# Kernel optimization log

Hardware: AMD Instinct MI355X
Metric: run time of the kernel (lower is better)

Reference implementation:

```python
import jax, jax.numpy as jnp
import numpy as np

SCALE = 1.0 / 4.0      # alpha / dim
MULTIPLIER = 1.0

def _act(h):
    return jax.nn.gelu(h, approximate=False)  # torch nn.GELU(approximate='none')

def setup_inputs() -> dict:
    key = jax.random.key(0)
    ks = jax.random.split(key, 9)
    B, T, D = 64, 77, 768
    N, R = 1024, 4
    return {
        "x":     jax.random.normal(ks[0], (B, T, D), jnp.float32),
        "W_org": jax.random.normal(ks[1], (D, D), jnp.float32) * 0.02,
        "b_org": jax.random.normal(ks[2], (D,), jnp.float32) * 0.02,
        "w1":    jax.random.normal(ks[3], (N, D, R), jnp.float32) * 0.02,
        "b1":    jax.random.normal(ks[4], (N, R), jnp.float32) * 0.02,
        "mid_w": jax.random.normal(ks[5], (N, R, R), jnp.float32) * 0.02,
        "mid_b": jax.random.normal(ks[6], (N, R), jnp.float32) * 0.02,
        "w_out": jax.random.normal(ks[7], (N, R, D), jnp.float32) * 0.02,
        "b_out": jax.random.normal(ks[8], (N, D), jnp.float32) * 0.02,
    }

def reference(x, W_org, b_org, w1, b1, mid_w, mid_b, w_out, b_out):
    # per-concept low-rank MLP: h in [B, T, N, R]
    h = jnp.einsum('btd,ndh->btnh', x, w1) + b1[None, None]
    h = _act(h)
    # repeated 'h' in 'nhh' takes the diagonal of mid_w (elementwise scale),
    # exactly matching torch.einsum semantics in the source.
    h = jnp.einsum('btnh,nhh->btnh', h, mid_w) + mid_b[None, None]
    h = _act(h)
    # fuse out-projection with sum over concepts: sum_n (h_n @ w_out_n) + sum_n b_out_n
    up = jnp.einsum('btnh,nhd->btd', h, w_out) + jnp.sum(b_out, axis=0)
    org = x @ W_org.T + b_org
    return org + up * (MULTIPLIER * SCALE)
```

## Files before the change

kernel.cpp:

```cpp
#include <hip/hip_runtime.h>
#include <hip/hip_bf16.h>

#define M_TOK 4928
#define M_PAD 5120
#define D_DIM 768
#define NR    4096
#define K_CAT 4864
#define KT_ALL 152

typedef __bf16 bf16;
typedef __attribute__((ext_vector_type(8))) __bf16 bf16x8;
typedef __attribute__((ext_vector_type(4))) float f32x4;
typedef __attribute__((address_space(1))) uint32_t gu32;
typedef __attribute__((address_space(3))) uint32_t su32;

#define GLDS(P, LDSP) \
  __builtin_amdgcn_global_load_lds((gu32*)(P), (su32*)(LDSP), 16, 0, 0)

__device__ __forceinline__ float act_fast(float v) {
  float e = __builtin_amdgcn_exp2f(v * -2.4554677f);
  return v * __builtin_amdgcn_rcpf(1.0f + e);
}

__device__ __forceinline__ int xcd_swizzle(int orig, int nwg) {
  const int q = nwg >> 3, r = nwg & 7;
  const int x = orig & 7, rest = orig >> 3;
  return (x < r ? x * (q + 1) : r * (q + 1) + (x - r) * q) + rest;
}


__global__ __launch_bounds__(256) void k_prep_x(const float* __restrict__ x,
                                                bf16* __restrict__ Xb) {
  int idx = (blockIdx.x * 256 + threadIdx.x) * 4;
  if (idx >= M_PAD * D_DIM) return;
  int m = idx / D_DIM;
  union { uint2 u; bf16 h[4]; } o;
  if (m < M_TOK) {
    float4 v = *(const float4*)(x + idx);
    o.h[0] = (bf16)v.x; o.h[1] = (bf16)v.y; o.h[2] = (bf16)v.z; o.h[3] = (bf16)v.w;
  } else {
    o.h[0] = o.h[1] = o.h[2] = o.h[3] = (bf16)0.0f;
  }
  *(uint2*)(Xb + idx) = o.u;
}

__global__ __launch_bounds__(256) void k_prep_w1t(const float* __restrict__ w1,
                                                  bf16* __restrict__ W1t) {
  int gid = blockIdx.x * 256 + threadIdx.x;
  int n = gid / 96, oct = gid % 96;
  const float4* src = (const float4*)w1 + (size_t)n * D_DIM + oct * 8;
  bf16x8 rows[4];
#pragma unroll
  for (int d = 0; d < 8; ++d) {
    float4 v = src[d];
    rows[0][d] = (bf16)v.x; rows[1][d] = (bf16)v.y;
    rows[2][d] = (bf16)v.z; rows[3][d] = (bf16)v.w;
  }
  size_t base = (size_t)n * 4 * D_DIM + oct * 8;
#pragma unroll
  for (int r = 0; r < 4; ++r)
    *(bf16x8*)(W1t + base + (size_t)r * D_DIM) = rows[r];
}

__global__ __launch_bounds__(256) void k_prep_w2t_t(const float* __restrict__ w_out,
                                                    bf16* __restrict__ W2t) {
  __shared__ float S[64 * 65];
  const int bk = blockIdx.x & 63, bd = blockIdx.x >> 6;
  const int k0 = bk * 64, d0 = bd * 64;
  const int tr = threadIdx.x >> 4;
  const int tc = (threadIdx.x & 15) * 4;
#pragma unroll
  for (int p = 0; p < 4; ++p) {
    const int kr = tr + p * 16;
    float4 v = *(const float4*)(w_out + (size_t)(k0 + kr) * D_DIM + d0 + tc);
    S[kr * 65 + tc + 0] = v.x; S[kr * 65 + tc + 1] = v.y;
    S[kr * 65 + tc + 2] = v.z; S[kr * 65 + tc + 3] = v.w;
  }
  __syncthreads();
#pragma unroll
  for (int p = 0; p < 4; ++p) {
    const int dr = tr + p * 16;
    union { uint2 u; bf16 h[4]; } o;
#pragma unroll
    for (int i = 0; i < 4; ++i) o.h[i] = (bf16)(0.25f * S[(tc + i) * 65 + dr]);
    *(uint2*)(W2t + (size_t)(d0 + dr) * K_CAT + k0 + tc) = o.u;
  }
}

__global__ __launch_bounds__(256) void k_prep_w2t_org(const float* __restrict__ W_org,
                                                      bf16* __restrict__ W2t) {
  int idx = (blockIdx.x * 256 + threadIdx.x) * 4;
  if (idx >= D_DIM * D_DIM) return;
  int d = idx / D_DIM, c = idx % D_DIM;
  float4 v = *(const float4*)(W_org + idx);
  union { uint2 u; bf16 h[4]; } o;
  o.h[0] = (bf16)v.x; o.h[1] = (bf16)v.y; o.h[2] = (bf16)v.z; o.h[3] = (bf16)v.w;
  *(uint2*)(W2t + (size_t)d * K_CAT + NR + c) = o.u;
}

__global__ __launch_bounds__(256) void k_bias_partial(const float* __restrict__ b_out,
                                                      float* __restrict__ partial) {
  int b = blockIdx.x;
  for (int d = threadIdx.x; d < D_DIM; d += 256) {
    float s = 0.0f;
    for (int n = b * 32; n < b * 32 + 32; ++n) s += b_out[n * D_DIM + d];
    partial[b * D_DIM + d] = s;
  }
}

__global__ __launch_bounds__(256) void k_bias_final2(const float* __restrict__ partial,
                                                     const float* __restrict__ b_org,
                                                     const float* __restrict__ mid_w,
                                                     float* __restrict__ bias_total,
                                                     float* __restrict__ diag) {
  int b = blockIdx.x;
  if (b < 3) {
    int d = b * 256 + threadIdx.x;
    if (d >= D_DIM) return;
    float s = 0.0f;
#pragma unroll
    for (int p = 0; p < 32; ++p) s += partial[p * D_DIM + d];
    bias_total[d] = b_org[d] + 0.25f * s;
  } else {
    int j = (b - 3) * 256 + threadIdx.x;
    diag[j] = mid_w[(j >> 2) * 16 + (j & 3) * 5];
  }
}


__device__ __forceinline__ int swz_slot(int kg, int lr) {
  return (kg ^ ((lr >> 1) & 3)) << 3;
}

__device__ __forceinline__ void stage_unit8(const bf16* g, int ld, int row0, int col0,
                                            bf16* lds) {
  const int lane = threadIdx.x & 63;
  const int wave = threadIdx.x >> 6;
  const int src_slot = (lane & 3) ^ ((lane >> 3) & 3);
#pragma unroll
  for (int c = 0; c < 2; ++c) {
    const int chunk = wave * 2 + c;
    const int row = row0 + chunk * 16 + (lane >> 2);
    const bf16* gp = g + (size_t)row * ld + col0 + (src_slot << 3);
    GLDS(gp, lds + chunk * 512);
  }
}

#define TILE_E (128 * 32)


#define G1_IT(S_, DO_STG, LAST_)                                                \
  {                                                                             \
    if (LAST_) { asm volatile("s_waitcnt vmcnt(0)" ::: "memory"); }             \
    else       { asm volatile("s_waitcnt vmcnt(4)" ::: "memory"); }             \
    asm volatile("s_barrier" ::: "memory");                                     \
    bf16x8 a_[4], b_[4];                                                        \
    _Pragma("unroll") for (int i = 0; i < 4; ++i)                               \
      a_[i] = *(const bf16x8*)(&As[S_][aOff + i * 512]);                        \
    _Pragma("unroll") for (int j = 0; j < 4; ++j)                               \
      b_[j] = *(const bf16x8*)(&Bs[S_][bOff + j * 512]);                        \
    if (DO_STG) {                                                               \
      GLDS(aP0, &As[((S_) + 2) % 3][ldsC0]);                                    \
      GLDS(aP1, &As[((S_) + 2) % 3][ldsC1]);                                    \
      GLDS(bP0, &Bs[((S_) + 2) % 3][ldsC0]);                                    \
      GLDS(bP1, &Bs[((S_) + 2) % 3][ldsC1]);                                    \
      aP0 += 32; aP1 += 32; bP0 += 32; bP1 += 32;                               \
    }                                                                           \
    _Pragma("unroll") for (int i = 0; i < 4; ++i)                               \
      _Pragma("unroll") for (int j = 0; j < 4; ++j)                             \
        acc[i][j] = __builtin_amdgcn_mfma_f32_16x16x32_bf16(b_[j], a_[i], acc[i][j], 0, 0, 0); \
  }

__global__ __launch_bounds__(256) void k_gemm1(const bf16* __restrict__ Xb,
                                               const bf16* __restrict__ W1t,
                                               bf16* __restrict__ H2,
                                               const float* __restrict__ b1,
                                               const float* __restrict__ diag,
                                               const float* __restrict__ midb) {
  __shared__ bf16 As[3][TILE_E];
  __shared__ bf16 Bs[3][TILE_E];
  const int wgid = xcd_swizzle(blockIdx.x, 39 * 32);
  const int bmt = wgid >> 5;
  const int bnt = wgid & 31;
  const int m0 = bmt * 128, n0 = bnt * 128;
  const int lane = threadIdx.x & 63;
  const int wave = threadIdx.x >> 6;
  const int wm = wave >> 1, wn = wave & 1;
  const int lr = lane & 15, kg = lane >> 4;
  const int slot = swz_slot(kg, lr);
  const int aOff = (wm * 64 + lr) * 32 + slot;
  const int bOff = (wn * 64 + lr) * 32 + slot;

  const int src_slot = (lane & 3) ^ ((lane >> 3) & 3);
  const int srow = (wave * 2) * 16 + (lane >> 2);
  const bf16* aP0 = Xb  + (size_t)(m0 + srow) * D_DIM + (src_slot << 3);
  const bf16* aP1 = aP0 + 16 * D_DIM;
  const bf16* bP0 = W1t + (size_t)(n0 + srow) * D_DIM + (src_slot << 3);
  const bf16* bP1 = bP0 + 16 * D_DIM;
  const int ldsC0 = (wave * 2) * 512, ldsC1 = ldsC0 + 512;

  f32x4 acc[4][4];
#pragma unroll
  for (int i = 0; i < 4; ++i)
#pragma unroll
    for (int j = 0; j < 4; ++j) acc[i][j] = (f32x4)(0.0f);

  GLDS(aP0, &As[0][ldsC0]); GLDS(aP1, &As[0][ldsC1]);
  GLDS(bP0, &Bs[0][ldsC0]); GLDS(bP1, &Bs[0][ldsC1]);
  aP0 += 32; aP1 += 32; bP0 += 32; bP1 += 32;
  GLDS(aP0, &As[1][ldsC0]); GLDS(aP1, &As[1][ldsC1]);
  GLDS(bP0, &Bs[1][ldsC0]); GLDS(bP1, &Bs[1][ldsC1]);
  aP0 += 32; aP1 += 32; bP0 += 32; bP1 += 32;

  for (int g = 0; g < 7; ++g) {
    G1_IT(0, true, false)
    G1_IT(1, true, false)
    G1_IT(2, true, false)
  }
  G1_IT(0, true, false)
  G1_IT(1, false, false)
  G1_IT(2, false, true)

#pragma unroll
  for (int j = 0; j < 4; ++j) {
    const int jcb = n0 + wn * 64 + j * 16 + kg * 4;
    const float4 b1v = *(const float4*)(b1 + jcb);
    const float4 dgv = *(const float4*)(diag + jcb);
    const float4 mbv = *(const float4*)(midb + jcb);
#pragma unroll
    for (int i = 0; i < 4; ++i) {
      const int mr = m0 + wm * 64 + i * 16 + lr;
      union { uint2 u; bf16 h[4]; } o;
      float h;
      h = act_fast(acc[i][j][0] + b1v.x); o.h[0] = (bf16)act_fast(h * dgv.x + mbv.x);
      h = act_fast(acc[i][j][1] + b1v.y); o.h[1] = (bf16)act_fast(h * dgv.y + mbv.y);
      h = act_fast(acc[i][j][2] + b1v.z); o.h[2] = (bf16)act_fast(h * dgv.z + mbv.z);
      h = act_fast(acc[i][j][3] + b1v.w); o.h[3] = (bf16)act_fast(h * dgv.w + mbv.w);
      *(uint2*)(H2 + (size_t)mr * NR + jcb) = o.u;
    }
  }
}


#define ENGINE(KT0, KT1, STAGE_A, STAGE_B)                                      \
  {                                                                             \
    STAGE_A((KT0) + 0, 0); STAGE_B((KT0) + 0, 0);                               \
    STAGE_A((KT0) + 1, 1); STAGE_B((KT0) + 1, 1);                               \
    STAGE_A((KT0) + 2, 2); STAGE_B((KT0) + 2, 2);                               \
    asm volatile("s_waitcnt vmcnt(8)" ::: "memory");                            \
    asm volatile("s_barrier" ::: "memory");                                     \
    for (int t = (KT0); t < (KT1); ++t) {                                       \
      const int s  = (t - (KT0)) & 3;                                           \
      const int st = (t - (KT0) + 3) & 3;                                       \
      const bool more = (t + 3 < (KT1));                                        \
      bf16x8 a[8], b[4];                                                        \
      _Pragma("unroll") for (int i = 0; i < 4; ++i)                             \
        a[i] = *(const bf16x8*)(As[s] + aBase + i * 512);                       \
      _Pragma("unroll") for (int j = 0; j < 4; ++j)                             \
        b[j] = *(const bf16x8*)(Bs[s] + bBase + j * 512);                       \
      if (more) { STAGE_A(t + 3, st); }                                         \
      asm volatile("s_barrier" ::: "memory");                                   \
      __builtin_amdgcn_s_setprio(1);                                            \
      _Pragma("unroll") for (int i = 0; i < 4; ++i)                             \
        _Pragma("unroll") for (int j = 0; j < 4; ++j)                           \
          acc[i][j] = __builtin_amdgcn_mfma_f32_16x16x32_bf16(b[j], a[i], acc[i][j], 0, 0, 0); \
      __builtin_amdgcn_s_setprio(0);                                            \
      asm volatile("s_barrier" ::: "memory");                                   \
      _Pragma("unroll") for (int i = 0; i < 4; ++i)                             \
        a[4 + i] = *(const bf16x8*)(As[s] + aBase + 2048 + i * 512);            \
      if (more) { STAGE_B(t + 3, st); }                                         \
      {                                                                         \
        int ahead = ((KT1) - 1) - (t + 1);                                      \
        if (ahead >= 2)      { asm volatile("s_waitcnt vmcnt(8)" ::: "memory"); } \
        else if (ahead == 1) { asm volatile("s_waitcnt vmcnt(4)" ::: "memory"); } \
        else                 { asm volatile("s_waitcnt vmcnt(0)" ::: "memory"); } \
      }                                                                         \
      asm volatile("s_barrier" ::: "memory");                                   \
      __builtin_amdgcn_s_setprio(1);                                            \
      _Pragma("unroll") for (int i = 0; i < 4; ++i)                             \
        _Pragma("unroll") for (int j = 0; j < 4; ++j)                           \
          acc[4 + i][j] = __builtin_amdgcn_mfma_f32_16x16x32_bf16(b[j], a[4 + i], acc[4 + i][j], 0, 0, 0); \
      __builtin_amdgcn_s_setprio(0);                                            \
      asm volatile("s_barrier" ::: "memory");                                   \
    }                                                                           \
  }

template <int SPLITS>
__global__ __launch_bounds__(512) void k_gemm2(const bf16* __restrict__ H2,
                                               const bf16* __restrict__ Xb,
                                               const bf16* __restrict__ W2t,
                                               void* __restrict__ outp,
                                               const float* __restrict__ bias) {
  __shared__ bf16 As[4][8192];
  __shared__ bf16 Bs[4][8192];
  const int nwg = 20 * 3 * SPLITS;
  const int wgid = xcd_swizzle(blockIdx.x, nwg);
  const int bmt = wgid / (3 * SPLITS);
  const int rem = wgid % (3 * SPLITS);
  const int ks  = rem / 3;
  const int bnt = rem % 3;
  const int m0 = bmt * 256, n0 = bnt * 256;
  const int lane = threadIdx.x & 63;
  const int wave = threadIdx.x >> 6;
  const int wm = wave >> 2, wn = wave & 3;
  const int lr = lane & 15, kg = lane >> 4;
  const int slotE = swz_slot(kg, lr);
  const int aBase = (wm * 128 + lr) * 32 + slotE;
  const int bBase = (wn * 64 + lr) * 32 + slotE;
  constexpr int KT_PER = KT_ALL / SPLITS;
  const int kt0 = ks * KT_PER, kt1 = kt0 + KT_PER;

  f32x4 acc[8][4];
#pragma unroll
  for (int i = 0; i < 8; ++i)
#pragma unroll
    for (int j = 0; j < 4; ++j) acc[i][j] = (f32x4)(0.0f);

#define G2_SA(kt, buf)                                                  \
  {                                                                     \
    const int k0s = (kt) * 32;                                          \
    if (k0s < NR) stage_unit8(H2, NR, m0, k0s, As[(buf)]);              \
    else          stage_unit8(Xb, D_DIM, m0, k0s - NR, As[(buf)]);      \
  }
#define G2_SB(kt, buf) stage_unit8(W2t, K_CAT, n0, (kt) * 32, Bs[(buf)])
  ENGINE(kt0, kt1, G2_SA, G2_SB)
#undef G2_SA
#undef G2_SB

  if (SPLITS > 1) {
    bf16* dst = (bf16*)outp + (size_t)ks * M_TOK * D_DIM;
#pragma unroll
    for (int j = 0; j < 4; ++j) {
      const int cb = n0 + wn * 64 + j * 16 + kg * 4;
#pragma unroll
      for (int i = 0; i < 8; ++i) {
        const int mr = m0 + wm * 128 + i * 16 + lr;
        if (mr < M_TOK) {
          union { uint2 u; bf16 h[4]; } o;
          o.h[0] = (bf16)acc[i][j][0]; o.h[1] = (bf16)acc[i][j][1];
          o.h[2] = (bf16)acc[i][j][2]; o.h[3] = (bf16)acc[i][j][3];
          *(uint2*)(dst + (size_t)mr * D_DIM + cb) = o.u;
        }
      }
    }
  } else {
    float* dst = (float*)outp;
#pragma unroll
    for (int j = 0; j < 4; ++j) {
      const int cb = n0 + wn * 64 + j * 16 + kg * 4;
      const f32x4 bv = *(const f32x4*)(bias + cb);
#pragma unroll
      for (int i = 0; i < 8; ++i) {
        const int mr = m0 + wm * 128 + i * 16 + lr;
        if (mr < M_TOK) {
          f32x4 o = acc[i][j] + bv;
          *(f32x4*)(dst + (size_t)mr * D_DIM + cb) = o;
        }
      }
    }
  }
}

template <int SPLITS>
__global__ __launch_bounds__(256) void k_reduce(const bf16* __restrict__ padd,
                                                const float* __restrict__ bias,
                                                float* __restrict__ out) {
  int idx = (blockIdx.x * 256 + threadIdx.x) * 4;
  if (idx >= M_TOK * D_DIM) return;
  float4 s = *(const float4*)(bias + (idx % D_DIM));
#pragma unroll
  for (int p = 0; p < SPLITS; ++p) {
    union { uint2 u; bf16 h[4]; } v;
    v.u = *(const uint2*)(padd + (size_t)p * M_TOK * D_DIM + idx);
    s.x += (float)v.h[0]; s.y += (float)v.h[1];
    s.z += (float)v.h[2]; s.w += (float)v.h[3];
  }
  *(float4*)(out + idx) = s;
}


extern "C" void kernel_launch(void* const* d_in, const int* in_sizes, int n_in,
                              void* d_out, int out_size, void* d_ws, size_t ws_size,
                              hipStream_t stream) {
  const float* x     = (const float*)d_in[0];
  const float* W_org = (const float*)d_in[1];
  const float* b_org = (const float*)d_in[2];
  const float* w1    = (const float*)d_in[3];
  const float* b1    = (const float*)d_in[4];
  const float* mid_w = (const float*)d_in[5];
  const float* mid_b = (const float*)d_in[6];
  const float* w_out = (const float*)d_in[7];
  const float* b_out = (const float*)d_in[8];
  float* out = (float*)d_out;

  bf16* Xb   = (bf16*)d_ws;
  bf16* W1t  = Xb  + (size_t)M_PAD * D_DIM;
  bf16* W2t  = W1t + (size_t)NR * D_DIM;
  bf16* H2   = W2t + (size_t)D_DIM * K_CAT;
  float* bias    = (float*)(H2 + (size_t)M_PAD * NR);
  float* partial = bias + 1024;
  float* diag    = partial + 32 * D_DIM;
  bf16* padd     = (bf16*)(diag + NR);

  const size_t base_bytes = (size_t)((char*)padd - (char*)d_ws);
  const size_t per_split  = (size_t)M_TOK * D_DIM * sizeof(bf16);
  int S = 1;
  if (ws_size >= base_bytes + 4 * per_split)      S = 4;
  else if (ws_size >= base_bytes + 2 * per_split) S = 2;

  k_prep_x     <<<(M_PAD * D_DIM / 4) / 256, 256, 0, stream>>>(x, Xb);
  k_prep_w1t   <<<384, 256, 0, stream>>>(w1, W1t);
  k_prep_w2t_t <<<64 * 12, 256, 0, stream>>>(w_out, W2t);
  k_prep_w2t_org<<<(D_DIM * D_DIM / 4 + 255) / 256, 256, 0, stream>>>(W_org, W2t);
  k_bias_partial<<<32, 256, 0, stream>>>(b_out, partial);
  k_bias_final2 <<<19, 256, 0, stream>>>(partial, b_org, mid_w, bias, diag);

  k_gemm1<<<39 * 32, 256, 0, stream>>>(Xb, W1t, H2, b1, diag, mid_b);

  const int red_grid = (M_TOK * D_DIM / 4 + 255) / 256;
  if (S == 4) {
    k_gemm2<4><<<20 * 3 * 4, 512, 0, stream>>>(H2, Xb, W2t, padd, bias);
    k_reduce<4><<<red_grid, 256, 0, stream>>>(padd, bias, out);
  } else if (S == 2) {
    k_gemm2<2><<<20 * 3 * 2, 512, 0, stream>>>(H2, Xb, W2t, padd, bias);
    k_reduce<2><<<red_grid, 256, 0, stream>>>(padd, bias, out);
  } else {
    k_gemm2<1><<<20 * 3, 512, 0, stream>>>(H2, Xb, W2t, out, bias);
  }
}
```

Before: 136.7 us.

## Run first GEMM in FP8 with scaled weights and quantized activations

Quantizes x and w1 (the latter pre-scaled by 64) to FP8 in new prep kernels and rewrites the first GEMM to use FP8 MFMA with 64-wide K tiles, halving the K-loop trip count and the bytes loaded per tile. The scale is undone in the epilogue. The cost is an extra prep kernel reading x again (the bf16 copy is still needed for the second GEMM) and reduced precision in the hidden activations, which may hurt accuracy.

```diff
diff --git a/kernel.cpp b/kernel.cpp
--- a/kernel.cpp
+++ b/kernel.cpp
@@ -9,6 +9,7 @@
 #define KT_ALL 152
 
 typedef __bf16 bf16;
+typedef unsigned char u8;
 typedef __attribute__((ext_vector_type(8))) __bf16 bf16x8;
 typedef __attribute__((ext_vector_type(4))) float f32x4;
 typedef __attribute__((address_space(1))) uint32_t gu32;
@@ -16,6 +17,13 @@
 
 #define GLDS(P, LDSP) \
   __builtin_amdgcn_global_load_lds((gu32*)(P), (su32*)(LDSP), 16, 0, 0)
+
+__device__ __forceinline__ uint32_t pk_fp8x4(float a, float b, float c, float d) {
+  uint32_t w = 0;
+  w = (uint32_t)__builtin_amdgcn_cvt_pk_fp8_f32(a, b, (int)w, false);
+  w = (uint32_t)__builtin_amdgcn_cvt_pk_fp8_f32(c, d, (int)w, true);
+  return w;
+}
 
 __device__ __forceinline__ float act_fast(float v) {
   float e = __builtin_amdgcn_exp2f(v * -2.4554677f);
@@ -44,22 +52,39 @@
   *(uint2*)(Xb + idx) = o.u;
 }
 
-__global__ __launch_bounds__(256) void k_prep_w1t(const float* __restrict__ w1,
-                                                  bf16* __restrict__ W1t) {
+__global__ __launch_bounds__(256) void k_prep_xq(const float* __restrict__ x,
+                                                 u8* __restrict__ Xq) {
+  int idx = (blockIdx.x * 256 + threadIdx.x) * 4;
+  if (idx >= M_PAD * D_DIM) return;
+  int m = idx / D_DIM;
+  uint32_t w = 0;
+  if (m < M_TOK) {
+    float4 v = *(const float4*)(x + idx);
+    w = pk_fp8x4(v.x, v.y, v.z, v.w);
+  }
+  *(uint32_t*)(Xq + idx) = w;
+}
+
+__global__ __launch_bounds__(256) void k_prep_w1q(const float* __restrict__ w1,
+                                                  u8* __restrict__ W1q) {
   int gid = blockIdx.x * 256 + threadIdx.x;
   int n = gid / 96, oct = gid % 96;
   const float4* src = (const float4*)w1 + (size_t)n * D_DIM + oct * 8;
-  bf16x8 rows[4];
+  float e[4][8];
 #pragma unroll
   for (int d = 0; d < 8; ++d) {
     float4 v = src[d];
-    rows[0][d] = (bf16)v.x; rows[1][d] = (bf16)v.y;
-    rows[2][d] = (bf16)v.z; rows[3][d] = (bf16)v.w;
+    e[0][d] = v.x * 64.0f; e[1][d] = v.y * 64.0f;
+    e[2][d] = v.z * 64.0f; e[3][d] = v.w * 64.0f;
   }
   size_t base = (size_t)n * 4 * D_DIM + oct * 8;
 #pragma unroll
-  for (int r = 0; r < 4; ++r)
-    *(bf16x8*)(W1t + base + (size_t)r * D_DIM) = rows[r];
+  for (int r = 0; r < 4; ++r) {
+    uint2 o;
+    o.x = pk_fp8x4(e[r][0], e[r][1], e[r][2], e[r][3]);
+    o.y = pk_fp8x4(e[r][4], e[r][5], e[r][6], e[r][7]);
+    *(uint2*)(W1q + base + (size_t)r * D_DIM) = o;
+  }
 }
 
 __global__ __launch_bounds__(256) void k_prep_w2t_t(const float* __restrict__ w_out,
@@ -146,39 +171,44 @@
   }
 }
 
-#define TILE_E (128 * 32)
-
-
-#define G1_IT(S_, DO_STG, LAST_)                                                \
+
+#define G1F_IT(S_, DO_STG, LAST_)                                               \
   {                                                                             \
     if (LAST_) { asm volatile("s_waitcnt vmcnt(0)" ::: "memory"); }             \
     else       { asm volatile("s_waitcnt vmcnt(4)" ::: "memory"); }             \
     asm volatile("s_barrier" ::: "memory");                                     \
-    bf16x8 a_[4], b_[4];                                                        \
-    _Pragma("unroll") for (int i = 0; i < 4; ++i)                               \
-      a_[i] = *(const bf16x8*)(&As[S_][aOff + i * 512]);                        \
-    _Pragma("unroll") for (int j = 0; j < 4; ++j)                               \
-      b_[j] = *(const bf16x8*)(&Bs[S_][bOff + j * 512]);                        \
+    long a0[4], a1[4], b0[4], b1[4];                                            \
+    _Pragma("unroll") for (int i = 0; i < 4; ++i) {                             \
+      a0[i] = *(const long*)(&As[S_][aOff + i * 1024]);                         \
+      a1[i] = *(const long*)(&As[S_][(aOff ^ 32) + i * 1024]);                  \
+    }                                                                           \
+    _Pragma("unroll") for (int j = 0; j < 4; ++j) {                             \
+      b0[j] = *(const long*)(&Bs[S_][bOff + j * 1024]);                         \
+      b1[j] = *(const long*)(&Bs[S_][(bOff ^ 32) + j * 1024]);                  \
+    }                                                                           \
     if (DO_STG) {                                                               \
       GLDS(aP0, &As[((S_) + 2) % 3][ldsC0]);                                    \
       GLDS(aP1, &As[((S_) + 2) % 3][ldsC1]);                                    \
       GLDS(bP0, &Bs[((S_) + 2) % 3][ldsC0]);                                    \
       GLDS(bP1, &Bs[((S_) + 2) % 3][ldsC1]);                                    \
-      aP0 += 32; aP1 += 32; bP0 += 32; bP1 += 32;                               \
+      aP0 += 64; aP1 += 64; bP0 += 64; bP1 += 64;                               \
     }                                                                           \
     _Pragma("unroll") for (int i = 0; i < 4; ++i)                               \
       _Pragma("unroll") for (int j = 0; j < 4; ++j)                             \
-        acc[i][j] = __builtin_amdgcn_mfma_f32_16x16x32_bf16(b_[j], a_[i], acc[i][j], 0, 0, 0); \
-  }
-
-__global__ __launch_bounds__(256) void k_gemm1(const bf16* __restrict__ Xb,
-                                               const bf16* __restrict__ W1t,
+        acc[i][j] = __builtin_amdgcn_mfma_f32_16x16x32_fp8_fp8(b0[j], a0[i], acc[i][j], 0, 0, 0); \
+    _Pragma("unroll") for (int i = 0; i < 4; ++i)                               \
+      _Pragma("unroll") for (int j = 0; j < 4; ++j)                             \
+        acc[i][j] = __builtin_amdgcn_mfma_f32_16x16x32_fp8_fp8(b1[j], a1[i], acc[i][j], 0, 0, 0); \
+  }
+
+__global__ __launch_bounds__(256) void k_gemm1(const u8* __restrict__ Xq,
+                                               const u8* __restrict__ W1q,
                                                bf16* __restrict__ H2,
                                                const float* __restrict__ b1,
                                                const float* __restrict__ diag,
                                                const float* __restrict__ midb) {
-  __shared__ bf16 As[3][TILE_E];
-  __shared__ bf16 Bs[3][TILE_E];
+  __shared__ u8 As[3][128 * 64];
+  __shared__ u8 Bs[3][128 * 64];
   const int wgid = xcd_swizzle(blockIdx.x, 39 * 32);
   const int bmt = wgid >> 5;
   const int bnt = wgid & 31;
@@ -187,17 +217,17 @@
   const int wave = threadIdx.x >> 6;
   const int wm = wave >> 1, wn = wave & 1;
   const int lr = lane & 15, kg = lane >> 4;
-  const int slot = swz_slot(kg, lr);
-  const int aOff = (wm * 64 + lr) * 32 + slot;
-  const int bOff = (wn * 64 + lr) * 32 + slot;
+  const int slotB = (((kg >> 1) ^ ((lr >> 1) & 3)) << 4) + ((kg & 1) << 3);
+  const int aOff = (wm * 64 + lr) * 64 + slotB;
+  const int bOff = (wn * 64 + lr) * 64 + slotB;
 
   const int src_slot = (lane & 3) ^ ((lane >> 3) & 3);
   const int srow = (wave * 2) * 16 + (lane >> 2);
-  const bf16* aP0 = Xb  + (size_t)(m0 + srow) * D_DIM + (src_slot << 3);
-  const bf16* aP1 = aP0 + 16 * D_DIM;
-  const bf16* bP0 = W1t + (size_t)(n0 + srow) * D_DIM + (src_slot << 3);
-  const bf16* bP1 = bP0 + 16 * D_DIM;
-  const int ldsC0 = (wave * 2) * 512, ldsC1 = ldsC0 + 512;
+  const u8* aP0 = Xq  + (size_t)(m0 + srow) * D_DIM + (src_slot << 4);
+  const u8* aP1 = aP0 + 16 * D_DIM;
+  const u8* bP0 = W1q + (size_t)(n0 + srow) * D_DIM + (src_slot << 4);
+  const u8* bP1 = bP0 + 16 * D_DIM;
+  const int ldsC0 = (wave * 2) * 1024, ldsC1 = ldsC0 + 1024;
 
   f32x4 acc[4][4];
 #pragma unroll
@@ -207,19 +237,19 @@
 
   GLDS(aP0, &As[0][ldsC0]); GLDS(aP1, &As[0][ldsC1]);
   GLDS(bP0, &Bs[0][ldsC0]); GLDS(bP1, &Bs[0][ldsC1]);
-  aP0 += 32; aP1 += 32; bP0 += 32; bP1 += 32;
+  aP0 += 64; aP1 += 64; bP0 += 64; bP1 += 64;
   GLDS(aP0, &As[1][ldsC0]); GLDS(aP1, &As[1][ldsC1]);
   GLDS(bP0, &Bs[1][ldsC0]); GLDS(bP1, &Bs[1][ldsC1]);
-  aP0 += 32; aP1 += 32; bP0 += 32; bP1 += 32;
-
-  for (int g = 0; g < 7; ++g) {
-    G1_IT(0, true, false)
-    G1_IT(1, true, false)
-    G1_IT(2, true, false)
-  }
-  G1_IT(0, true, false)
-  G1_IT(1, false, false)
-  G1_IT(2, false, true)
+  aP0 += 64; aP1 += 64; bP0 += 64; bP1 += 64;
+
+  for (int g = 0; g < 3; ++g) {
+    G1F_IT(0, true, false)
+    G1F_IT(1, true, false)
+    G1F_IT(2, true, false)
+  }
+  G1F_IT(0, true, false)
+  G1F_IT(1, false, false)
+  G1F_IT(2, false, true)
 
 #pragma unroll
   for (int j = 0; j < 4; ++j) {
@@ -232,10 +262,10 @@
       const int mr = m0 + wm * 64 + i * 16 + lr;
       union { uint2 u; bf16 h[4]; } o;
       float h;
-      h = act_fast(acc[i][j][0] + b1v.x); o.h[0] = (bf16)act_fast(h * dgv.x + mbv.x);
-      h = act_fast(acc[i][j][1] + b1v.y); o.h[1] = (bf16)act_fast(h * dgv.y + mbv.y);
-      h = act_fast(acc[i][j][2] + b1v.z); o.h[2] = (bf16)act_fast(h * dgv.z + mbv.z);
-      h = act_fast(acc[i][j][3] + b1v.w); o.h[3] = (bf16)act_fast(h * dgv.w + mbv.w);
+      h = act_fast(fmaf(acc[i][j][0], 0.015625f, b1v.x)); o.h[0] = (bf16)act_fast(h * dgv.x + mbv.x);
+      h = act_fast(fmaf(acc[i][j][1], 0.015625f, b1v.y)); o.h[1] = (bf16)act_fast(h * dgv.y + mbv.y);
+      h = act_fast(fmaf(acc[i][j][2], 0.015625f, b1v.z)); o.h[2] = (bf16)act_fast(h * dgv.z + mbv.z);
+      h = act_fast(fmaf(acc[i][j][3], 0.015625f, b1v.w)); o.h[3] = (bf16)act_fast(h * dgv.w + mbv.w);
       *(uint2*)(H2 + (size_t)mr * NR + jcb) = o.u;
     }
   }
@@ -394,13 +424,14 @@
   float* out = (float*)d_out;
 
   bf16* Xb   = (bf16*)d_ws;
-  bf16* W1t  = Xb  + (size_t)M_PAD * D_DIM;
-  bf16* W2t  = W1t + (size_t)NR * D_DIM;
+  bf16* W2t  = Xb  + (size_t)M_PAD * D_DIM;
   bf16* H2   = W2t + (size_t)D_DIM * K_CAT;
   float* bias    = (float*)(H2 + (size_t)M_PAD * NR);
   float* partial = bias + 1024;
   float* diag    = partial + 32 * D_DIM;
-  bf16* padd     = (bf16*)(diag + NR);
+  u8*   Xq   = (u8*)(diag + NR);
+  u8*   W1q  = Xq + (size_t)M_PAD * D_DIM;
+  bf16* padd = (bf16*)(W1q + (size_t)NR * D_DIM);
 
   const size_t base_bytes = (size_t)((char*)padd - (char*)d_ws);
   const size_t per_split  = (size_t)M_TOK * D_DIM * sizeof(bf16);
@@ -408,14 +439,15 @@
   if (ws_size >= base_bytes + 4 * per_split)      S = 4;
   else if (ws_size >= base_bytes + 2 * per_split) S = 2;
 
-  k_prep_x     <<<(M_PAD * D_DIM / 4) / 256, 256, 0, stream>>>(x, Xb);
-  k_prep_w1t   <<<384, 256, 0, stream>>>(w1, W1t);
-  k_prep_w2t_t <<<64 * 12, 256, 0, stream>>>(w_out, W2t);
+  k_prep_x      <<<(M_PAD * D_DIM / 4) / 256, 256, 0, stream>>>(x, Xb);
+  k_prep_xq     <<<(M_PAD * D_DIM / 4) / 256, 256, 0, stream>>>(x, Xq);
+  k_prep_w1q    <<<384, 256, 0, stream>>>(w1, W1q);
+  k_prep_w2t_t  <<<64 * 12, 256, 0, stream>>>(w_out, W2t);
   k_prep_w2t_org<<<(D_DIM * D_DIM / 4 + 255) / 256, 256, 0, stream>>>(W_org, W2t);
   k_bias_partial<<<32, 256, 0, stream>>>(b_out, partial);
   k_bias_final2 <<<19, 256, 0, stream>>>(partial, b_org, mid_w, bias, diag);
 
-  k_gemm1<<<39 * 32, 256, 0, stream>>>(Xb, W1t, H2, b1, diag, mid_b);
+  k_gemm1<<<39 * 32, 256, 0, stream>>>(Xq, W1q, H2, b1, diag, mid_b);
 
   const int red_grid = (M_TOK * D_DIM / 4 + 255) / 256;
   if (S == 4) {
```

Measured after the change: 118.9 us. 13.0% less time.
